# Kernel optimization log

Measured on AMD Instinct MI355X. Metric: run time of the kernel, lower is better.

Reference implementation:

```python
import jax, jax.numpy as jnp
import numpy as np

M_BUCKETS = 2048  # input_features // q = 4096 // 2


def countsketch(x, hash_idx, rand_sgn, m=M_BUCKETS):
    # x: [N, D]; scatter-add signed columns into m buckets -> [N, m]
    return jnp.zeros((x.shape[0], m), x.dtype).at[:, hash_idx].add(x * rand_sgn[None, :])


def setup_inputs() -> dict:
    key = jax.random.key(0)
    k1, k2, k3, k4, k5 = jax.random.split(key, 5)
    B, D, O = 4096, 4096, 4096
    inp = jax.random.normal(k1, (B, D), dtype=jnp.float32)
    # match torch init: weight uniform(-sqrt(3)/sqrt(D), sqrt(3)/sqrt(D)), bias uniform(-1/sqrt(D), 1/sqrt(D))
    bound = 1.0 / np.sqrt(D)
    weight = jax.random.uniform(k2, (O, D), dtype=jnp.float32,
                                minval=-bound * np.sqrt(3.0), maxval=bound * np.sqrt(3.0))
    bias = jax.random.uniform(k3, (O,), dtype=jnp.float32, minval=-bound, maxval=bound)
    hash_idx = jax.random.randint(k4, (D,), 0, M_BUCKETS, dtype=jnp.int32)
    rand_sgn = (2.0 * jax.random.randint(k5, (D,), 0, 2).astype(jnp.float32) - 1.0)
    return {"input": inp, "weight": weight, "bias": bias,
            "hash_idx": hash_idx, "rand_sgn": rand_sgn}


def reference(input, weight, bias, hash_idx, rand_sgn):
    input_sketch = countsketch(input, hash_idx, rand_sgn)    # [B, m]
    weight_sketch = countsketch(weight, hash_idx, rand_sgn)  # [O, m]
    out = input_sketch @ weight_sketch.T + bias[None, :]     # [B, O]
    return out
```

## Files before the change

kernel.cpp:

```cpp
#include <hip/hip_runtime.h>
#include <hip/hip_bf16.h>
#include <stdint.h>

#define D_DIM     4096
#define MB        2048
#define NROWS     4096
#define K_DIM     MB

typedef __bf16 bf16x8 __attribute__((ext_vector_type(8)));
typedef float  floatx4 __attribute__((ext_vector_type(4)));

__device__ __forceinline__ void gld_lds16(const void* g, void* l) {
    __builtin_amdgcn_global_load_lds(
        (const __attribute__((address_space(1))) unsigned int*)g,
        (__attribute__((address_space(3))) unsigned int*)l,
        16, 0, 0);
}

__global__ __launch_bounds__(256) void build_csr(
    const int* __restrict__ hash_idx,
    unsigned int* __restrict__ desc,
    unsigned short* __restrict__ cols16)
{
    __shared__ int cnt[MB];
    __shared__ int scan[MB];
    const int t = threadIdx.x;

    for (int k = t; k < MB; k += 256) cnt[k] = 0;
    __syncthreads();
    for (int j = t; j < D_DIM; j += 256) atomicAdd(&cnt[hash_idx[j]], 1);
    __syncthreads();
    for (int k = t; k < MB; k += 256) scan[k] = cnt[k];
    __syncthreads();
    for (int stride = 1; stride < MB; stride <<= 1) {
        int vals[8];
        #pragma unroll
        for (int i = 0; i < 8; ++i) {
            int k = t + 256 * i;
            vals[i] = (k >= stride) ? scan[k - stride] : 0;
        }
        __syncthreads();
        #pragma unroll
        for (int i = 0; i < 8; ++i) scan[t + 256 * i] += vals[i];
        __syncthreads();
    }
    for (int k = t; k < MB; k += 256) {
        int excl = scan[k] - cnt[k];
        desc[k] = ((unsigned)excl << 5) | (unsigned)cnt[k];
        cnt[k] = excl;
    }
    __syncthreads();
    for (int j = t; j < D_DIM; j += 256) {
        int k = hash_idx[j];
        int pos = atomicAdd(&cnt[k], 1);
        cols16[pos] = (unsigned short)j;
    }
}

__global__ __launch_bounds__(256) void sketch2(
    const float* __restrict__ input,
    const float* __restrict__ weight,
    const float* __restrict__ rand_sgn,
    const unsigned int* __restrict__ desc,
    const unsigned short* __restrict__ cols16,
    __hip_bfloat16* __restrict__ sk_in,
    __hip_bfloat16* __restrict__ sk_w)
{
    __shared__ float rowAB[2 * D_DIM];
    __shared__ __align__(16) unsigned short cols[D_DIM];
    const int b = blockIdx.x;
    const bool is_w = (b >= NROWS / 2);
    const int pr = is_w ? (b - NROWS / 2) : b;
    const float* src = (is_w ? weight : input) + (size_t)pr * 2 * D_DIM;
    __hip_bfloat16* dst = (is_w ? sk_w : sk_in) + (size_t)pr * 2 * MB;
    const int t = threadIdx.x;

    gld_lds16(cols16 + t * 8,         &cols[t * 8]);
    gld_lds16(cols16 + (t + 256) * 8, &cols[(t + 256) * 8]);

    const float4* s4 = (const float4*)src;
    const float4* g4 = (const float4*)rand_sgn;
    float4* r4 = (float4*)rowAB;
    #pragma unroll
    for (int p = 0; p < 8; ++p) {
        int idx = t + 256 * p;
        float4 x = s4[idx];
        float4 g = g4[idx & 1023];
        float4 y; y.x = x.x * g.x; y.y = x.y * g.y; y.z = x.z * g.z; y.w = x.w * g.w;
        r4[idx] = y;
    }
    __syncthreads();

    #pragma unroll
    for (int i = 0; i < 8; ++i) {
        int k = t + 256 * i;
        unsigned d = desc[k];
        int st = (int)(d >> 5), c = (int)(d & 31);
        float s0 = 0.f, s1 = 0.f;
        for (int p = 0; p < c; ++p) {
            int j = cols[st + p];
            s0 += rowAB[j];
            s1 += rowAB[D_DIM + j];
        }
        dst[k]      = __float2bfloat16(s0);
        dst[MB + k] = __float2bfloat16(s1);
    }
}

__global__ __launch_bounds__(256) void gemm_bt_bias(
    const __hip_bfloat16* __restrict__ A,
    const __hip_bfloat16* __restrict__ B,
    const float* __restrict__ bias,
    float* __restrict__ C)
{
    __shared__ __align__(16) __hip_bfloat16 lA[128 * 64];
    __shared__ __align__(16) __hip_bfloat16 lB[128 * 64];

    const int t = threadIdx.x;
    const int lane = t & 63;
    const int wid  = t >> 6;
    const int warpM = wid & 1, warpN = wid >> 1;
    const int quad = lane >> 4;
    const int mrow = lane & 15;
    const int rowBase = blockIdx.y * 128;
    const int colBase = blockIdx.x * 128;

    const __hip_bfloat16* gA[4];
    const __hip_bfloat16* gB[4];
    #pragma unroll
    for (int p = 0; p < 4; ++p) {
        int G = t + 256 * p;
        int m = G >> 3;
        int q = (G & 7) ^ (m & 7);
        gA[p] = A + (size_t)(rowBase + m) * K_DIM + q * 8;
        gB[p] = B + (size_t)(colBase + m) * K_DIM + q * 8;
    }
    __hip_bfloat16* sA = &lA[t * 8];
    __hip_bfloat16* sB = &lB[t * 8];

    floatx4 acc[4][4];
    const floatx4 zero = {0.f, 0.f, 0.f, 0.f};
    #pragma unroll
    for (int i = 0; i < 4; ++i)
        #pragma unroll
        for (int j = 0; j < 4; ++j) acc[i][j] = zero;

    for (int kb = 0; kb < K_DIM; kb += 64) {
        #pragma unroll
        for (int p = 0; p < 4; ++p) {
            gld_lds16(gA[p] + kb, sA + p * 2048);
            gld_lds16(gB[p] + kb, sB + p * 2048);
        }
        __syncthreads();

        #pragma unroll
        for (int h = 0; h < 2; ++h) {
            bf16x8 af[4], bfr[4];
            #pragma unroll
            for (int i = 0; i < 4; ++i) {
                int mA = warpM * 64 + i * 16 + mrow;
                int sa = (h * 4 + quad) ^ (mA & 7);
                af[i] = *(const bf16x8*)&lA[(mA * 8 + sa) * 8];
                int mB = warpN * 64 + i * 16 + mrow;
                int sb = (h * 4 + quad) ^ (mB & 7);
                bfr[i] = *(const bf16x8*)&lB[(mB * 8 + sb) * 8];
            }
            #pragma unroll
            for (int i = 0; i < 4; ++i)
                #pragma unroll
                for (int j = 0; j < 4; ++j)
                    acc[i][j] = __builtin_amdgcn_mfma_f32_16x16x32_bf16(
                        af[i], bfr[j], acc[i][j], 0, 0, 0);
        }
        __syncthreads();
    }

    float bj[4];
    #pragma unroll
    for (int j = 0; j < 4; ++j) bj[j] = bias[colBase + warpN * 64 + j * 16 + mrow];
    #pragma unroll
    for (int i = 0; i < 4; ++i) {
        int m0 = rowBase + warpM * 64 + i * 16 + quad * 4;
        #pragma unroll
        for (int j = 0; j < 4; ++j) {
            int n = colBase + warpN * 64 + j * 16 + mrow;
            #pragma unroll
            for (int p = 0; p < 4; ++p)
                C[(size_t)(m0 + p) * NROWS + n] = acc[i][j][p] + bj[j];
        }
    }
}

extern "C" void kernel_launch(void* const* d_in, const int* in_sizes, int n_in,
                              void* d_out, int out_size, void* d_ws, size_t ws_size,
                              hipStream_t stream) {
    const float* input  = (const float*)d_in[0];
    const float* weight = (const float*)d_in[1];
    const float* bias   = (const float*)d_in[2];
    const int*   hidx   = (const int*)d_in[3];
    const float* sgn    = (const float*)d_in[4];
    float* out = (float*)d_out;

    char* ws = (char*)d_ws;
    __hip_bfloat16* sk_in = (__hip_bfloat16*)ws;
    __hip_bfloat16* sk_w  = (__hip_bfloat16*)(ws + (size_t)16 * 1024 * 1024);
    unsigned int*   desc  = (unsigned int*)(ws + (size_t)32 * 1024 * 1024);
    unsigned short* cols16 = (unsigned short*)(ws + (size_t)32 * 1024 * 1024 + 8192);

    build_csr<<<1, 256, 0, stream>>>(hidx, desc, cols16);
    sketch2<<<NROWS, 256, 0, stream>>>(input, weight, sgn, desc, cols16,
                                       sk_in, sk_w);
    gemm_bt_bias<<<dim3(32, 32), 256, 0, stream>>>(sk_in, sk_w, bias, out);
}
```

Baseline: 268.6 us.

## Replace CSR gather sketch with LDS atomic scatter, dropping build_csr kernel

Removes the single-block CSR construction kernel and the gather-based sketch, replacing them with a kernel where each block handles four rows and scatters signed values into LDS buckets using shared-memory float atomics. This eliminates a serial one-block launch and the dependent index loads in the gather. In exchange, LDS atomics may contend on bank and bucket collisions, and the order of the float additions becomes nondeterministic.

```diff
diff --git a/kernel.cpp b/kernel.cpp
--- a/kernel.cpp
+++ b/kernel.cpp
@@ -17,93 +17,62 @@
         16, 0, 0);
 }
 
-__global__ __launch_bounds__(256) void build_csr(
-    const int* __restrict__ hash_idx,
-    unsigned int* __restrict__ desc,
-    unsigned short* __restrict__ cols16)
-{
-    __shared__ int cnt[MB];
-    __shared__ int scan[MB];
-    const int t = threadIdx.x;
-
-    for (int k = t; k < MB; k += 256) cnt[k] = 0;
-    __syncthreads();
-    for (int j = t; j < D_DIM; j += 256) atomicAdd(&cnt[hash_idx[j]], 1);
-    __syncthreads();
-    for (int k = t; k < MB; k += 256) scan[k] = cnt[k];
-    __syncthreads();
-    for (int stride = 1; stride < MB; stride <<= 1) {
-        int vals[8];
-        #pragma unroll
-        for (int i = 0; i < 8; ++i) {
-            int k = t + 256 * i;
-            vals[i] = (k >= stride) ? scan[k - stride] : 0;
-        }
-        __syncthreads();
-        #pragma unroll
-        for (int i = 0; i < 8; ++i) scan[t + 256 * i] += vals[i];
-        __syncthreads();
-    }
-    for (int k = t; k < MB; k += 256) {
-        int excl = scan[k] - cnt[k];
-        desc[k] = ((unsigned)excl << 5) | (unsigned)cnt[k];
-        cnt[k] = excl;
-    }
-    __syncthreads();
-    for (int j = t; j < D_DIM; j += 256) {
-        int k = hash_idx[j];
-        int pos = atomicAdd(&cnt[k], 1);
-        cols16[pos] = (unsigned short)j;
-    }
-}
-
-__global__ __launch_bounds__(256) void sketch2(
+__global__ __launch_bounds__(256) void sketch_scatter(
     const float* __restrict__ input,
     const float* __restrict__ weight,
     const float* __restrict__ rand_sgn,
-    const unsigned int* __restrict__ desc,
-    const unsigned short* __restrict__ cols16,
+    const int* __restrict__ hash_idx,
     __hip_bfloat16* __restrict__ sk_in,
     __hip_bfloat16* __restrict__ sk_w)
 {
-    __shared__ float rowAB[2 * D_DIM];
-    __shared__ __align__(16) unsigned short cols[D_DIM];
+    __shared__ float bkt[4 * MB];
     const int b = blockIdx.x;
-    const bool is_w = (b >= NROWS / 2);
-    const int pr = is_w ? (b - NROWS / 2) : b;
-    const float* src = (is_w ? weight : input) + (size_t)pr * 2 * D_DIM;
-    __hip_bfloat16* dst = (is_w ? sk_w : sk_in) + (size_t)pr * 2 * MB;
+    const bool is_w = (b >= NROWS / 4);
+    const int qr = is_w ? (b - NROWS / 4) : b;
+    const float* src = (is_w ? weight : input) + (size_t)qr * 4 * D_DIM;
+    __hip_bfloat16* dst = (is_w ? sk_w : sk_in) + (size_t)qr * 4 * MB;
     const int t = threadIdx.x;
 
-    gld_lds16(cols16 + t * 8,         &cols[t * 8]);
-    gld_lds16(cols16 + (t + 256) * 8, &cols[(t + 256) * 8]);
+    float4* b4 = (float4*)bkt;
+    const float4 z4 = {0.f, 0.f, 0.f, 0.f};
+    #pragma unroll
+    for (int i = 0; i < 8; ++i) b4[t + 256 * i] = z4;
+    __syncthreads();
 
-    const float4* s4 = (const float4*)src;
-    const float4* g4 = (const float4*)rand_sgn;
-    float4* r4 = (float4*)rowAB;
+    const float4* src4 = (const float4*)src;
+    const float4* g4   = (const float4*)rand_sgn;
+    const int4*   h4   = (const int4*)hash_idx;
     #pragma unroll
-    for (int p = 0; p < 8; ++p) {
+    for (int p = 0; p < 4; ++p) {
         int idx = t + 256 * p;
-        float4 x = s4[idx];
-        float4 g = g4[idx & 1023];
-        float4 y; y.x = x.x * g.x; y.y = x.y * g.y; y.z = x.z * g.z; y.w = x.w * g.w;
-        r4[idx] = y;
+        int4   h = h4[idx];
+        float4 s = g4[idx];
+        #pragma unroll
+        for (int r = 0; r < 4; ++r) {
+            float4 x = src4[(size_t)r * 1024 + idx];
+            float* bk = &bkt[r * MB];
+            atomicAdd(&bk[h.x], x.x * s.x);
+            atomicAdd(&bk[h.y], x.y * s.y);
+            atomicAdd(&bk[h.z], x.z * s.z);
+            atomicAdd(&bk[h.w], x.w * s.w);
+        }
     }
     __syncthreads();
 
     #pragma unroll
-    for (int i = 0; i < 8; ++i) {
-        int k = t + 256 * i;
-        unsigned d = desc[k];
-        int st = (int)(d >> 5), c = (int)(d & 31);
-        float s0 = 0.f, s1 = 0.f;
-        for (int p = 0; p < c; ++p) {
-            int j = cols[st + p];
-            s0 += rowAB[j];
-            s1 += rowAB[D_DIM + j];
+    for (int r = 0; r < 4; ++r) {
+        unsigned* drow = (unsigned*)(dst + (size_t)r * MB);
+        const float2* brow = (const float2*)&bkt[r * MB];
+        #pragma unroll
+        for (int i = 0; i < 4; ++i) {
+            int kk = t + 256 * i;
+            float2 v = brow[kk];
+            __hip_bfloat16 b0 = __float2bfloat16(v.x);
+            __hip_bfloat16 b1 = __float2bfloat16(v.y);
+            unsigned u = (unsigned)*(unsigned short*)&b0 |
+                         ((unsigned)*(unsigned short*)&b1 << 16);
+            drow[kk] = u;
         }
-        dst[k]      = __float2bfloat16(s0);
-        dst[MB + k] = __float2bfloat16(s1);
     }
 }
 
@@ -204,11 +173,8 @@
     char* ws = (char*)d_ws;
     __hip_bfloat16* sk_in = (__hip_bfloat16*)ws;
     __hip_bfloat16* sk_w  = (__hip_bfloat16*)(ws + (size_t)16 * 1024 * 1024);
-    unsigned int*   desc  = (unsigned int*)(ws + (size_t)32 * 1024 * 1024);
-    unsigned short* cols16 = (unsigned short*)(ws + (size_t)32 * 1024 * 1024 + 8192);
 
-    build_csr<<<1, 256, 0, stream>>>(hidx, desc, cols16);
-    sketch2<<<NROWS, 256, 0, stream>>>(input, weight, sgn, desc, cols16,
-                                       sk_in, sk_w);
+    sketch_scatter<<<2 * (NROWS / 4), 256, 0, stream>>>(
+        input, weight, sgn, hidx, sk_in, sk_w);
     gemm_bt_bias<<<dim3(32, 32), 256, 0, stream>>>(sk_in, sk_w, bias, out);
 }
```

New measurement: 358.6 us. +33.5%, slower.

## Permute sketch rows in LDS so bucket sums read contiguous entries

Applied to the files above, without the earlier changes.

The sketch kernel now gathers each signed row into bucket-sorted order in LDS using the CSR permutation, then sums contiguous runs per bucket with a fixed 8-wide predicated unrolled loop plus a tail. This replaces the old per-element indirect column lookup inside a variable-length loop, cutting dependent LDS index loads and divergence. It adds an extra LDS pass with two more barriers, and the descriptor encoding is widened to 16 bits.

```diff
diff --git a/kernel.cpp b/kernel.cpp
--- a/kernel.cpp
+++ b/kernel.cpp
@@ -20,7 +20,7 @@
 __global__ __launch_bounds__(256) void build_csr(
     const int* __restrict__ hash_idx,
     unsigned int* __restrict__ desc,
-    unsigned short* __restrict__ cols16)
+    unsigned short* __restrict__ perm16)
 {
     __shared__ int cnt[MB];
     __shared__ int scan[MB];
@@ -46,28 +46,29 @@
     }
     for (int k = t; k < MB; k += 256) {
         int excl = scan[k] - cnt[k];
-        desc[k] = ((unsigned)excl << 5) | (unsigned)cnt[k];
+        desc[k] = ((unsigned)excl << 16) | (unsigned)cnt[k];
         cnt[k] = excl;
     }
     __syncthreads();
     for (int j = t; j < D_DIM; j += 256) {
         int k = hash_idx[j];
         int pos = atomicAdd(&cnt[k], 1);
-        cols16[pos] = (unsigned short)j;
-    }
-}
-
-__global__ __launch_bounds__(256) void sketch2(
+        perm16[pos] = (unsigned short)j;
+    }
+}
+
+__global__ __launch_bounds__(256) void sketch_gather(
     const float* __restrict__ input,
     const float* __restrict__ weight,
     const float* __restrict__ rand_sgn,
     const unsigned int* __restrict__ desc,
-    const unsigned short* __restrict__ cols16,
+    const unsigned short* __restrict__ perm16,
     __hip_bfloat16* __restrict__ sk_in,
     __hip_bfloat16* __restrict__ sk_w)
 {
-    __shared__ float rowAB[2 * D_DIM];
-    __shared__ __align__(16) unsigned short cols[D_DIM];
+    __shared__ __align__(16) float rv0[D_DIM + 8];
+    __shared__ __align__(16) float rv1[D_DIM + 8];
+    __shared__ __align__(16) unsigned short perm[D_DIM];
     const int b = blockIdx.x;
     const bool is_w = (b >= NROWS / 2);
     const int pr = is_w ? (b - NROWS / 2) : b;
@@ -75,19 +76,40 @@
     __hip_bfloat16* dst = (is_w ? sk_w : sk_in) + (size_t)pr * 2 * MB;
     const int t = threadIdx.x;
 
-    gld_lds16(cols16 + t * 8,         &cols[t * 8]);
-    gld_lds16(cols16 + (t + 256) * 8, &cols[(t + 256) * 8]);
+    const uint4* pg = (const uint4*)perm16;
+    ((uint4*)perm)[t]       = pg[t];
+    ((uint4*)perm)[t + 256] = pg[t + 256];
 
     const float4* s4 = (const float4*)src;
     const float4* g4 = (const float4*)rand_sgn;
-    float4* r4 = (float4*)rowAB;
-    #pragma unroll
-    for (int p = 0; p < 8; ++p) {
-        int idx = t + 256 * p;
-        float4 x = s4[idx];
-        float4 g = g4[idx & 1023];
-        float4 y; y.x = x.x * g.x; y.y = x.y * g.y; y.z = x.z * g.z; y.w = x.w * g.w;
-        r4[idx] = y;
+    #pragma unroll
+    for (int i = 0; i < 4; ++i) {
+        int q = t + 256 * i;
+        float4 g = g4[q];
+        float4 x0 = s4[q], x1 = s4[q + 1024];
+        float4 y0; y0.x = x0.x*g.x; y0.y = x0.y*g.y; y0.z = x0.z*g.z; y0.w = x0.w*g.w;
+        float4 y1; y1.x = x1.x*g.x; y1.y = x1.y*g.y; y1.z = x1.z*g.z; y1.w = x1.w*g.w;
+        *(float4*)&rv0[4 * q] = y0;
+        *(float4*)&rv1[4 * q] = y1;
+    }
+    __syncthreads();
+
+    float4 a0[4], a1[4];
+    #pragma unroll
+    for (int i = 0; i < 4; ++i) {
+        int q = t + 256 * i;
+        ushort4 pp = *(const ushort4*)&perm[4 * q];
+        a0[i].x = rv0[pp.x]; a0[i].y = rv0[pp.y];
+        a0[i].z = rv0[pp.z]; a0[i].w = rv0[pp.w];
+        a1[i].x = rv1[pp.x]; a1[i].y = rv1[pp.y];
+        a1[i].z = rv1[pp.z]; a1[i].w = rv1[pp.w];
+    }
+    __syncthreads();
+    #pragma unroll
+    for (int i = 0; i < 4; ++i) {
+        int q = t + 256 * i;
+        *(float4*)&rv0[4 * q] = a0[i];
+        *(float4*)&rv1[4 * q] = a1[i];
     }
     __syncthreads();
 
@@ -95,12 +117,17 @@
     for (int i = 0; i < 8; ++i) {
         int k = t + 256 * i;
         unsigned d = desc[k];
-        int st = (int)(d >> 5), c = (int)(d & 31);
+        int st = (int)(d >> 16), c = (int)(d & 0xFFFF);
         float s0 = 0.f, s1 = 0.f;
-        for (int p = 0; p < c; ++p) {
-            int j = cols[st + p];
-            s0 += rowAB[j];
-            s1 += rowAB[D_DIM + j];
+        #pragma unroll
+        for (int j = 0; j < 8; ++j) {
+            float v0 = rv0[st + j], v1 = rv1[st + j];
+            bool m = (j < c);
+            s0 += m ? v0 : 0.f;
+            s1 += m ? v1 : 0.f;
+        }
+        for (int j = 8; j < c; ++j) {
+            s0 += rv0[st + j]; s1 += rv1[st + j];
         }
         dst[k]      = __float2bfloat16(s0);
         dst[MB + k] = __float2bfloat16(s1);
@@ -205,10 +232,10 @@
     __hip_bfloat16* sk_in = (__hip_bfloat16*)ws;
     __hip_bfloat16* sk_w  = (__hip_bfloat16*)(ws + (size_t)16 * 1024 * 1024);
     unsigned int*   desc  = (unsigned int*)(ws + (size_t)32 * 1024 * 1024);
-    unsigned short* cols16 = (unsigned short*)(ws + (size_t)32 * 1024 * 1024 + 8192);
-
-    build_csr<<<1, 256, 0, stream>>>(hidx, desc, cols16);
-    sketch2<<<NROWS, 256, 0, stream>>>(input, weight, sgn, desc, cols16,
-                                       sk_in, sk_w);
+    unsigned short* perm16 = (unsigned short*)(ws + (size_t)32 * 1024 * 1024 + 8192);
+
+    build_csr<<<1, 256, 0, stream>>>(hidx, desc, perm16);
+    sketch_gather<<<NROWS, 256, 0, stream>>>(input, weight, sgn, desc, perm16,
+                                             sk_in, sk_w);
     gemm_bt_bias<<<dim3(32, 32), 256, 0, stream>>>(sk_in, sk_w, bias, out);
 }
```

Measured after the change: 261.8 us. -2.6%, faster.
